# Kernel optimization log

Measured on AMD Instinct MI355X. Metric: run time of the kernel, lower is better.

The kernel has to match this reference:

```python
import jax, jax.numpy as jnp
import numpy as np

N, E, H, C = 50000, 800000, 4, 32   # nodes, edges, heads, per-head channels
HID, LAT, G = H * C, 32, 128        # hidden, latent, num graphs
IN_DIM = 64
NEG_SLOPE = 0.2
BN_EPS = 1e-5


def setup_inputs() -> dict:
    key = jax.random.key(0)
    ks = jax.random.split(key, 20)
    inp = {
        "x": jax.random.normal(ks[0], (N, IN_DIM), jnp.float32),
        "edge_index": jax.random.randint(ks[1], (2, E), 0, N, jnp.int32),
        "batch": jnp.sort(jax.random.randint(ks[2], (N,), 0, G, jnp.int32)),
        # layer 0
        "W0": jax.random.normal(ks[3], (IN_DIM, HID), jnp.float32) * (1.0 / np.sqrt(IN_DIM)),
        "a_src0": jax.random.normal(ks[4], (H, C), jnp.float32) * 0.1,
        "a_dst0": jax.random.normal(ks[5], (H, C), jnp.float32) * 0.1,
        "b0": jnp.zeros((HID,), jnp.float32),
        # layer 1
        "W1": jax.random.normal(ks[6], (HID, HID), jnp.float32) * (1.0 / np.sqrt(HID)),
        "a_src1": jax.random.normal(ks[7], (H, C), jnp.float32) * 0.1,
        "a_dst1": jax.random.normal(ks[8], (H, C), jnp.float32) * 0.1,
        "b1": jnp.zeros((HID,), jnp.float32),
        # layer 2
        "W2": jax.random.normal(ks[9], (HID, HID), jnp.float32) * (1.0 / np.sqrt(HID)),
        "a_src2": jax.random.normal(ks[10], (H, C), jnp.float32) * 0.1,
        "a_dst2": jax.random.normal(ks[11], (H, C), jnp.float32) * 0.1,
        "b2": jnp.zeros((HID,), jnp.float32),
        # head
        "fc_w": jax.random.normal(ks[12], (HID, LAT), jnp.float32) * (1.0 / np.sqrt(HID)),
        "fc_b": jnp.zeros((LAT,), jnp.float32),
        "bn_g": jnp.ones((LAT,), jnp.float32),
        "bn_b": jnp.zeros((LAT,), jnp.float32),
    }
    return inp


def _gat_conv(x, src, dst, W, a_src, a_dst, b):
    n = x.shape[0]
    h = (x @ W).reshape(n, H, C)                      # [N,H,C]
    alpha_s = jnp.einsum("nhc,hc->nh", h, a_src)       # [N,H]
    alpha_d = jnp.einsum("nhc,hc->nh", h, a_dst)
    e = jax.nn.leaky_relu(alpha_s[src] + alpha_d[dst], NEG_SLOPE)  # [E',H]
    # scatter-softmax over incoming edges of each dst node
    m = jax.ops.segment_max(e, dst, num_segments=n)
    m = jnp.where(jnp.isfinite(m), m, 0.0)
    ex = jnp.exp(e - m[dst])
    denom = jax.ops.segment_sum(ex, dst, num_segments=n)
    alpha = ex / (denom[dst] + 1e-16)                  # [E',H]
    out = jax.ops.segment_sum(alpha[:, :, None] * h[src], dst, num_segments=n)
    return out.reshape(n, H * C) + b


def reference(x, edge_index, batch, W0, a_src0, a_dst0, b0, W1, a_src1, a_dst1, b1,
              W2, a_src2, a_dst2, b2, fc_w, fc_b, bn_g, bn_b):
    # PyG GATConv default add_self_loops=True
    loop = jnp.arange(N, dtype=edge_index.dtype)
    src = jnp.concatenate([edge_index[0], loop])
    dst = jnp.concatenate([edge_index[1], loop])

    h = x
    for (W, a_s, a_d, b) in ((W0, a_src0, a_dst0, b0),
                             (W1, a_src1, a_dst1, b1),
                             (W2, a_src2, a_dst2, b2)):
        h = _gat_conv(h, src, dst, W, a_s, a_d, b)
        h = jax.nn.leaky_relu(h, NEG_SLOPE)  # dropout is identity in eval

    pooled = jax.ops.segment_sum(h, batch, num_segments=G)  # global_add_pool -> [G,HID]
    out = pooled @ fc_w + fc_b
    # BatchNorm1d in eval mode with running_mean=0, running_var=1
    out = bn_g * out * (1.0 / np.sqrt(1.0 + BN_EPS)) + bn_b
    return out
```

## Files before the change

kernel.cpp:

```cpp
#include <hip/hip_runtime.h>
#include <hip/hip_bf16.h>
#include <float.h>

#define NEG 0.2f
#define SEGSHIFT 13
#define KE 24

__device__ __forceinline__ float leaky(float x) { return x > 0.0f ? x : NEG * x; }

__device__ __forceinline__ unsigned short f2bf(float f) {
  unsigned x = __float_as_uint(f);
  unsigned r = (x + 0x7fffu + ((x >> 16) & 1u)) >> 16;
  return (unsigned short)r;
}

__device__ __forceinline__ float2 bf2f2(unsigned u) {
  float2 r;
  r.x = __uint_as_float(u << 16);
  r.y = __uint_as_float(u & 0xffff0000u);
  return r;
}

using frag8 = __attribute__((ext_vector_type(8))) short;
using f32x4v = __attribute__((ext_vector_type(4))) float;

__global__ void zero_kernel(int* __restrict__ p, int n) {
  int i = blockIdx.x * blockDim.x + threadIdx.x;
  int stride = gridDim.x * blockDim.x;
  for (; i < n; i += stride) p[i] = 0;
}

__global__ void wcvt_kernel(const float* __restrict__ W, unsigned short* __restrict__ Wt, int K) {
  int i = blockIdx.x * 256 + threadIdx.x;
  if (i >= K * 128) return;
  int k = i >> 7, n = i & 127;
  Wt[n * K + k] = f2bf(W[i]);
}

__global__ void count_kernel(const int* __restrict__ ei, int* __restrict__ degseg,
                             int E, int N, int nseg) {
  int i = blockIdx.x * blockDim.x + threadIdx.x;
  if (i >= E + N) return;
  int src, dst;
  if (i < E) { src = ei[i]; dst = ei[E + i]; } else { src = dst = i - E; }
  atomicAdd(&degseg[(size_t)dst * nseg + (src >> SEGSHIFT)], 1);
}

__global__ __launch_bounds__(1024) void scan_block_kernel(const int* __restrict__ deg,
                                                          int* __restrict__ row_start,
                                                          int* __restrict__ sums, int n) {
  __shared__ int buf[1024];
  int t = threadIdx.x;
  int idx = blockIdx.x * 1024 + t;
  int x = (idx < n) ? deg[idx] : 0;
  int v = x;
  buf[t] = v;
  __syncthreads();
  for (int off = 1; off < 1024; off <<= 1) {
    int a = (t >= off) ? buf[t - off] : 0;
    __syncthreads();
    v += a;
    buf[t] = v;
    __syncthreads();
  }
  if (idx < n) row_start[idx] = v - x;
  if (t == 1023) sums[blockIdx.x] = v;
}

__global__ __launch_bounds__(1024) void scan_sums_kernel(int* __restrict__ sums,
                                                         int* __restrict__ row_start,
                                                         int nch, int n) {
  __shared__ int buf[1024];
  int t = threadIdx.x;
  int x = (t < nch) ? sums[t] : 0;
  int v = x;
  buf[t] = v;
  __syncthreads();
  for (int off = 1; off < 1024; off <<= 1) {
    int a = (t >= off) ? buf[t - off] : 0;
    __syncthreads();
    v += a;
    buf[t] = v;
    __syncthreads();
  }
  if (t < nch) sums[t] = v - x;
  if (t == 1023) row_start[n] = v;
}

__global__ __launch_bounds__(1024) void scan_add_kernel(int* __restrict__ row_start,
                                                        const int* __restrict__ sums, int n) {
  int idx = blockIdx.x * 1024 + threadIdx.x;
  if (idx < n) row_start[idx] += sums[blockIdx.x];
}

__global__ void fill_kernel(const int* __restrict__ ei, int* __restrict__ cursor,
                            const int* __restrict__ rowseg, int* __restrict__ csr_src,
                            int E, int N, int nseg) {
  int i = blockIdx.x * blockDim.x + threadIdx.x;
  if (i >= E + N) return;
  int src, dst;
  if (i < E) { src = ei[i]; dst = ei[E + i]; } else { src = dst = i - E; }
  size_t b = (size_t)dst * nseg + (src >> SEGSHIFT);
  int pos = atomicAdd(&cursor[b], 1);
  csr_src[rowseg[b] + pos] = src;
}

template <int FP32IN>
__global__ __launch_bounds__(256) void gemm_kernel(const void* __restrict__ Xin,
                                                   const unsigned short* __restrict__ Wtg,
                                                   unsigned short* __restrict__ Hb,
                                                   const float* __restrict__ a_src,
                                                   const float* __restrict__ a_dst,
                                                   float* __restrict__ as_arr,
                                                   float* __restrict__ ad_arr,
                                                   int nrows, int K) {
  __shared__ unsigned short Wt[128][136];
  __shared__ unsigned short Xs[64][136];
  int t = threadIdx.x;
  int wave = t >> 6, lane = t & 63;
  int n0 = lane & 15, quad = lane >> 4;
  int row0 = blockIdx.x * 64, wrow = wave * 16;

  for (int idx = t; idx < (K * 128) / 8; idx += 256) {
    int n = idx / (K >> 3), c8 = idx % (K >> 3);
    *(uint4*)(&Wt[n][c8 * 8]) = *(const uint4*)(Wtg + (size_t)n * K + c8 * 8);
  }
  int rowElems = K >> 3;
  if (FP32IN) {
    const float* Xf = (const float*)Xin;
    for (int idx = t; idx < 64 * K; idx += 256) {
      int r = idx / K, k = idx % K;
      int gr = row0 + r;
      Xs[r][k] = f2bf(gr < nrows ? Xf[(size_t)gr * K + k] : 0.f);
    }
  } else {
    const unsigned short* Xb = (const unsigned short*)Xin;
    for (int idx = t; idx < 64 * rowElems; idx += 256) {
      int r = idx / rowElems, c8 = idx % rowElems;
      int gr = row0 + r;
      uint4 v = make_uint4(0, 0, 0, 0);
      if (gr < nrows) v = *(const uint4*)(Xb + (size_t)gr * K + c8 * 8);
      *(uint4*)(&Xs[r][c8 * 8]) = v;
    }
  }
  __syncthreads();

  f32x4v acc[8];
#pragma unroll
  for (int c = 0; c < 8; ++c) acc[c] = (f32x4v){0.f, 0.f, 0.f, 0.f};

  for (int kb = 0; kb < K; kb += 32) {
    frag8 a = *(const frag8*)(&Xs[wrow + n0][kb + quad * 8]);
#pragma unroll
    for (int c = 0; c < 8; ++c) {
      frag8 b = *(const frag8*)(&Wt[c * 16 + n0][kb + quad * 8]);
      acc[c] = __builtin_amdgcn_mfma_f32_16x16x32_bf16(a, b, acc[c], 0, 0, 0);
    }
  }

  float asv[8], adv[8];
#pragma unroll
  for (int c = 0; c < 8; ++c) {
    asv[c] = a_src[c * 16 + n0];
    adv[c] = a_dst[c * 16 + n0];
  }
#pragma unroll
  for (int r = 0; r < 4; ++r) {
    float ps[4] = {0.f, 0.f, 0.f, 0.f}, pd[4] = {0.f, 0.f, 0.f, 0.f};
#pragma unroll
    for (int c = 0; c < 8; ++c) {
      int h = c >> 1;
      ps[h] += acc[c][r] * asv[c];
      pd[h] += acc[c][r] * adv[c];
    }
#pragma unroll
    for (int off = 1; off < 16; off <<= 1) {
#pragma unroll
      for (int h = 0; h < 4; ++h) {
        ps[h] += __shfl_xor(ps[h], off);
        pd[h] += __shfl_xor(pd[h], off);
      }
    }
    if (n0 == 0) {
      int m = row0 + wrow + quad * 4 + r;
      if (m < nrows) {
#pragma unroll
        for (int h = 0; h < 4; ++h) {
          as_arr[(size_t)m * 4 + h] = ps[h];
          ad_arr[(size_t)m * 4 + h] = pd[h];
        }
      }
    }
  }

  __syncthreads();
#pragma unroll
  for (int c = 0; c < 8; ++c)
#pragma unroll
    for (int r = 0; r < 4; ++r)
      Xs[wrow + quad * 4 + r][c * 16 + n0] = f2bf(acc[c][r]);
  __syncthreads();
  for (int idx = t; idx < 64 * 16; idx += 256) {
    int r = idx >> 4, c8 = idx & 15;
    int gr = row0 + r;
    if (gr < nrows)
      *(uint4*)(Hb + (size_t)gr * 128 + c8 * 8) = *(const uint4*)(&Xs[r][c8 * 8]);
  }
}

template <int POOL>
__global__ __launch_bounds__(256) void agg_kernel(const unsigned short* __restrict__ Hb,
                                                  const float* __restrict__ as_arr,
                                                  const float* __restrict__ ad_arr,
                                                  const int* __restrict__ csr_src,
                                                  const int* __restrict__ rowseg,
                                                  const float* __restrict__ bias,
                                                  unsigned short* __restrict__ xnext,
                                                  const int* __restrict__ batch,
                                                  float* __restrict__ pooled,
                                                  int N, int nseg) {
  __shared__ __align__(16) char rowbuf[4][KE * 256];
  __shared__ __align__(16) float e_lds[4][KE][4];
  int wid = threadIdx.x >> 6;
  int lane = threadIdx.x & 63;
  int n = blockIdx.x * 4 + wid;
  if (n >= N) return;
  int rs = rowseg[(size_t)n * nseg];
  int re = rowseg[(size_t)n * nseg + nseg];
  int l16 = lane & 15;
  int sub = lane >> 4;
  int head = l16 >> 2;

  float4 ad4 = *(const float4*)(ad_arr + (size_t)n * 4);
  char* myrows = rowbuf[wid];

  float4 dsum = make_float4(0.f, 0.f, 0.f, 0.f);
  float acc[8];
#pragma unroll
  for (int c = 0; c < 8; ++c) acc[c] = 0.f;

  for (int base = rs; base < re; base += KE) {
    asm volatile("s_waitcnt lgkmcnt(0)" ::: "memory");

    int sj = 0;
    float4 e4 = make_float4(0.f, 0.f, 0.f, 0.f);
    if (lane < KE && base + lane < re) {
      sj = csr_src[base + lane];
      float4 a4 = *(const float4*)(as_arr + (size_t)sj * 4);
      e4.x = __expf(fminf(leaky(a4.x + ad4.x), 80.f));
      e4.y = __expf(fminf(leaky(a4.y + ad4.y), 80.f));
      e4.z = __expf(fminf(leaky(a4.z + ad4.z), 80.f));
      e4.w = __expf(fminf(leaky(a4.w + ad4.w), 80.f));
      dsum.x += e4.x; dsum.y += e4.y; dsum.z += e4.z; dsum.w += e4.w;
    }
    if (lane < KE) *(float4*)(&e_lds[wid][lane][0]) = e4;

#pragma unroll
    for (int j = 0; j < KE; ++j) {
      int sju = __builtin_amdgcn_readlane(sj, j);
      const char* gp = (const char*)Hb + (size_t)(unsigned)sju * 256 + lane * 4;
      __builtin_amdgcn_global_load_lds(
          (const __attribute__((address_space(1))) void*)gp,
          (__attribute__((address_space(3))) void*)(myrows + j * 256), 4, 0, 0);
    }
    asm volatile("s_waitcnt vmcnt(0) lgkmcnt(0)" ::: "memory");
    __builtin_amdgcn_sched_barrier(0);

#pragma unroll
    for (int j = 0; j < KE; j += 4) {
      float w = e_lds[wid][j + sub][head];
      uint4 u = *(const uint4*)(myrows + (j + sub) * 256 + l16 * 16);
      float2 f;
      f = bf2f2(u.x); acc[0] += w * f.x; acc[1] += w * f.y;
      f = bf2f2(u.y); acc[2] += w * f.x; acc[3] += w * f.y;
      f = bf2f2(u.z); acc[4] += w * f.x; acc[5] += w * f.y;
      f = bf2f2(u.w); acc[6] += w * f.x; acc[7] += w * f.y;
    }
  }

#pragma unroll
  for (int c = 0; c < 8; ++c) acc[c] += __shfl_xor(acc[c], 16);
#pragma unroll
  for (int c = 0; c < 8; ++c) acc[c] += __shfl_xor(acc[c], 32);

#pragma unroll
  for (int off = 1; off < 64; off <<= 1) {
    dsum.x += __shfl_xor(dsum.x, off);
    dsum.y += __shfl_xor(dsum.y, off);
    dsum.z += __shfl_xor(dsum.z, off);
    dsum.w += __shfl_xor(dsum.w, off);
  }
  float denom = (head == 0) ? dsum.x : (head == 1) ? dsum.y : (head == 2) ? dsum.z : dsum.w;
  float inv = 1.0f / (denom + 1e-16f);

  if (POOL) {
    int g = batch[n];
    float p0 = 0.f, p1 = 0.f;
    switch (sub) {
      case 0: p0 = acc[0]; p1 = acc[1]; break;
      case 1: p0 = acc[2]; p1 = acc[3]; break;
      case 2: p0 = acc[4]; p1 = acc[5]; break;
      case 3: p0 = acc[6]; p1 = acc[7]; break;
    }
    int ch = 8 * l16 + 2 * sub;
    float v0 = leaky(p0 * inv + bias[ch]);
    float v1 = leaky(p1 * inv + bias[ch + 1]);
    atomicAdd(&pooled[(size_t)g * 128 + ch], v0);
    atomicAdd(&pooled[(size_t)g * 128 + ch + 1], v1);
  } else {
    if (sub == 0) {
      float4 bv0 = *(const float4*)(bias + 8 * l16);
      float4 bv1 = *(const float4*)(bias + 8 * l16 + 4);
      float v0 = leaky(acc[0] * inv + bv0.x);
      float v1 = leaky(acc[1] * inv + bv0.y);
      float v2 = leaky(acc[2] * inv + bv0.z);
      float v3 = leaky(acc[3] * inv + bv0.w);
      float v4 = leaky(acc[4] * inv + bv1.x);
      float v5 = leaky(acc[5] * inv + bv1.y);
      float v6 = leaky(acc[6] * inv + bv1.z);
      float v7 = leaky(acc[7] * inv + bv1.w);
      uint4 pk;
      pk.x = ((unsigned)f2bf(v1) << 16) | (unsigned)f2bf(v0);
      pk.y = ((unsigned)f2bf(v3) << 16) | (unsigned)f2bf(v2);
      pk.z = ((unsigned)f2bf(v5) << 16) | (unsigned)f2bf(v4);
      pk.w = ((unsigned)f2bf(v7) << 16) | (unsigned)f2bf(v6);
      ((uint4*)xnext)[(size_t)n * 16 + l16] = pk;
    }
  }
}

__global__ void head_kernel(const float* __restrict__ pooled, const float* __restrict__ fc_w,
                            const float* __restrict__ fc_b, const float* __restrict__ bn_g,
                            const float* __restrict__ bn_b, float* __restrict__ out, int G) {
  int t = threadIdx.x;
  int g = blockIdx.x * 8 + (t >> 5);
  int j = t & 31;
  if (g >= G) return;
  const float* pr = pooled + (size_t)g * 128;
  float acc = 0.f;
#pragma unroll 8
  for (int k = 0; k < 128; ++k) acc += pr[k] * fc_w[k * 32 + j];
  const float inv = 0.9999950000374997f;
  out[g * 32 + j] = bn_g[j] * (acc + fc_b[j]) * inv + bn_b[j];
}

extern "C" void kernel_launch(void* const* d_in, const int* in_sizes, int n_in,
                              void* d_out, int out_size, void* d_ws, size_t ws_size,
                              hipStream_t stream) {
  const float* x = (const float*)d_in[0];
  const int* ei = (const int*)d_in[1];
  const int* batch = (const int*)d_in[2];
  const float* Wm[3] = {(const float*)d_in[3], (const float*)d_in[7], (const float*)d_in[11]};
  const float* a_s[3] = {(const float*)d_in[4], (const float*)d_in[8], (const float*)d_in[12]};
  const float* a_d[3] = {(const float*)d_in[5], (const float*)d_in[9], (const float*)d_in[13]};
  const float* bb[3] = {(const float*)d_in[6], (const float*)d_in[10], (const float*)d_in[14]};
  const float* fc_w = (const float*)d_in[15];
  const float* fc_b = (const float*)d_in[16];
  const float* bn_g = (const float*)d_in[17];
  const float* bn_b = (const float*)d_in[18];
  float* out = (float*)d_out;

  int N = in_sizes[0] / 64;
  int E = in_sizes[1] / 2;
  int G = out_size / 32;
  int Etot = E + N;
  int nseg = ((N - 1) >> SEGSHIFT) + 1;
  int L = N * nseg;

  char* p = (char*)d_ws;
  auto carve = [&](size_t bytes) {
    char* r = p;
    p += (bytes + 255) & ~size_t(255);
    return r;
  };
  int* degseg    = (int*)carve((size_t)L * 4);
  int* cursor    = (int*)carve((size_t)L * 4);
  float* pooled  = (float*)carve((size_t)G * 128 * 4);
  int* rowseg    = (int*)carve((size_t)(L + 1) * 4);
  int* sums      = (int*)carve(4096);
  int* csr_src   = (int*)carve((size_t)Etot * 4);
  unsigned short* Hb  = (unsigned short*)carve((size_t)N * 128 * 2);
  unsigned short* Xb  = (unsigned short*)carve((size_t)N * 128 * 2);
  unsigned short* Wt0 = (unsigned short*)carve(64 * 128 * 2);
  unsigned short* Wt1 = (unsigned short*)carve(128 * 128 * 2);
  unsigned short* Wt2 = (unsigned short*)carve(128 * 128 * 2);
  float* as_arr  = (float*)carve((size_t)N * 4 * 4);
  float* ad_arr  = (float*)carve((size_t)N * 4 * 4);

  int nz = (int)(((char*)(pooled + (size_t)G * 128) - (char*)degseg) / 4);
  zero_kernel<<<512, 256, 0, stream>>>(degseg, nz);

  wcvt_kernel<<<(64 * 128 + 255) / 256, 256, 0, stream>>>(Wm[0], Wt0, 64);
  wcvt_kernel<<<(128 * 128 + 255) / 256, 256, 0, stream>>>(Wm[1], Wt1, 128);
  wcvt_kernel<<<(128 * 128 + 255) / 256, 256, 0, stream>>>(Wm[2], Wt2, 128);

  int egrid = (Etot + 255) / 256;
  count_kernel<<<egrid, 256, 0, stream>>>(ei, degseg, E, N, nseg);
  int nch = (L + 1023) / 1024;
  scan_block_kernel<<<nch, 1024, 0, stream>>>(degseg, rowseg, sums, L);
  scan_sums_kernel<<<1, 1024, 0, stream>>>(sums, rowseg, nch, L);
  scan_add_kernel<<<nch, 1024, 0, stream>>>(rowseg, sums, L);
  fill_kernel<<<egrid, 256, 0, stream>>>(ei, cursor, rowseg, csr_src, E, N, nseg);

  int ggrid = (N + 63) / 64;
  int ngrid = (N + 3) / 4;

  gemm_kernel<1><<<ggrid, 256, 0, stream>>>(x, Wt0, Hb, a_s[0], a_d[0], as_arr, ad_arr, N, 64);
  agg_kernel<0><<<ngrid, 256, 0, stream>>>(Hb, as_arr, ad_arr, csr_src, rowseg, bb[0],
                                           Xb, nullptr, nullptr, N, nseg);
  gemm_kernel<0><<<ggrid, 256, 0, stream>>>(Xb, Wt1, Hb, a_s[1], a_d[1], as_arr, ad_arr, N, 128);
  agg_kernel<0><<<ngrid, 256, 0, stream>>>(Hb, as_arr, ad_arr, csr_src, rowseg, bb[1],
                                           Xb, nullptr, nullptr, N, nseg);
  gemm_kernel<0><<<ggrid, 256, 0, stream>>>(Xb, Wt2, Hb, a_s[2], a_d[2], as_arr, ad_arr, N, 128);
  agg_kernel<1><<<ngrid, 256, 0, stream>>>(Hb, as_arr, ad_arr, csr_src, rowseg, bb[2],
                                           nullptr, batch, pooled, N, nseg);

  head_kernel<<<(G + 7) / 8, 256, 0, stream>>>(pooled, fc_w, fc_b, bn_g, bn_b, out, G);
}
```

Before: 502.3 us.

## Replace LDS-staged row gathers with direct vector loads in GAT aggregation

The aggregation kernel stops staging neighbour feature rows into shared memory with global_load_lds and per-batch waitcnt barriers. Each wave now walks 16 edges at a time, broadcasts source indices and attention weights through lane shuffles, and issues four direct 16-byte global loads per lane. This removes the LDS traffic, the buffers and the full-drain waits. It also raises occupancy through a launch-bounds hint, at the cost of smaller batches per iteration and more shuffle instructions.

```diff
diff --git a/kernel.cpp b/kernel.cpp
--- a/kernel.cpp
+++ b/kernel.cpp
@@ -4,7 +4,6 @@
 
 #define NEG 0.2f
 #define SEGSHIFT 13
-#define KE 24
 
 __device__ __forceinline__ float leaky(float x) { return x > 0.0f ? x : NEG * x; }
 
@@ -208,19 +207,34 @@
   }
 }
 
+#define COMPG(E, U)                                                 \
+  do {                                                              \
+    float2 f_;                                                      \
+    f_ = bf2f2((U).x); acc[0] += (E) * f_.x; acc[1] += (E) * f_.y;  \
+    f_ = bf2f2((U).y); acc[2] += (E) * f_.x; acc[3] += (E) * f_.y;  \
+    f_ = bf2f2((U).z); acc[4] += (E) * f_.x; acc[5] += (E) * f_.y;  \
+    f_ = bf2f2((U).w); acc[6] += (E) * f_.x; acc[7] += (E) * f_.y;  \
+  } while (0)
+
+__device__ __forceinline__ float eselect(const float4& e4, int src, int head) {
+  float x = __shfl(e4.x, src);
+  float y = __shfl(e4.y, src);
+  float z = __shfl(e4.z, src);
+  float w = __shfl(e4.w, src);
+  return head == 0 ? x : head == 1 ? y : head == 2 ? z : w;
+}
+
 template <int POOL>
-__global__ __launch_bounds__(256) void agg_kernel(const unsigned short* __restrict__ Hb,
-                                                  const float* __restrict__ as_arr,
-                                                  const float* __restrict__ ad_arr,
-                                                  const int* __restrict__ csr_src,
-                                                  const int* __restrict__ rowseg,
-                                                  const float* __restrict__ bias,
-                                                  unsigned short* __restrict__ xnext,
-                                                  const int* __restrict__ batch,
-                                                  float* __restrict__ pooled,
-                                                  int N, int nseg) {
-  __shared__ __align__(16) char rowbuf[4][KE * 256];
-  __shared__ __align__(16) float e_lds[4][KE][4];
+__global__ __launch_bounds__(256, 4) void agg_kernel(const unsigned short* __restrict__ Hb,
+                                                     const float* __restrict__ as_arr,
+                                                     const float* __restrict__ ad_arr,
+                                                     const int* __restrict__ csr_src,
+                                                     const int* __restrict__ rowseg,
+                                                     const float* __restrict__ bias,
+                                                     unsigned short* __restrict__ xnext,
+                                                     const int* __restrict__ batch,
+                                                     float* __restrict__ pooled,
+                                                     int N, int nseg) {
   int wid = threadIdx.x >> 6;
   int lane = threadIdx.x & 63;
   int n = blockIdx.x * 4 + wid;
@@ -232,50 +246,42 @@
   int head = l16 >> 2;
 
   float4 ad4 = *(const float4*)(ad_arr + (size_t)n * 4);
-  char* myrows = rowbuf[wid];
+  const uint4* hb4 = (const uint4*)Hb;
 
   float4 dsum = make_float4(0.f, 0.f, 0.f, 0.f);
   float acc[8];
 #pragma unroll
   for (int c = 0; c < 8; ++c) acc[c] = 0.f;
 
-  for (int base = rs; base < re; base += KE) {
-    asm volatile("s_waitcnt lgkmcnt(0)" ::: "memory");
-
-    int sj = 0;
+  for (int i = rs; i < re; i += 16) {
+    int cnt = re - i;
+    int sld = 0;
     float4 e4 = make_float4(0.f, 0.f, 0.f, 0.f);
-    if (lane < KE && base + lane < re) {
-      sj = csr_src[base + lane];
-      float4 a4 = *(const float4*)(as_arr + (size_t)sj * 4);
+    if (lane < 16 && lane < cnt) {
+      sld = csr_src[i + lane];
+      float4 a4 = *(const float4*)(as_arr + (size_t)sld * 4);
       e4.x = __expf(fminf(leaky(a4.x + ad4.x), 80.f));
       e4.y = __expf(fminf(leaky(a4.y + ad4.y), 80.f));
       e4.z = __expf(fminf(leaky(a4.z + ad4.z), 80.f));
       e4.w = __expf(fminf(leaky(a4.w + ad4.w), 80.f));
       dsum.x += e4.x; dsum.y += e4.y; dsum.z += e4.z; dsum.w += e4.w;
     }
-    if (lane < KE) *(float4*)(&e_lds[wid][lane][0]) = e4;
-
-#pragma unroll
-    for (int j = 0; j < KE; ++j) {
-      int sju = __builtin_amdgcn_readlane(sj, j);
-      const char* gp = (const char*)Hb + (size_t)(unsigned)sju * 256 + lane * 4;
-      __builtin_amdgcn_global_load_lds(
-          (const __attribute__((address_space(1))) void*)gp,
-          (__attribute__((address_space(3))) void*)(myrows + j * 256), 4, 0, 0);
-    }
-    asm volatile("s_waitcnt vmcnt(0) lgkmcnt(0)" ::: "memory");
-    __builtin_amdgcn_sched_barrier(0);
-
-#pragma unroll
-    for (int j = 0; j < KE; j += 4) {
-      float w = e_lds[wid][j + sub][head];
-      uint4 u = *(const uint4*)(myrows + (j + sub) * 256 + l16 * 16);
-      float2 f;
-      f = bf2f2(u.x); acc[0] += w * f.x; acc[1] += w * f.y;
-      f = bf2f2(u.y); acc[2] += w * f.x; acc[3] += w * f.y;
-      f = bf2f2(u.z); acc[4] += w * f.x; acc[5] += w * f.y;
-      f = bf2f2(u.w); acc[6] += w * f.x; acc[7] += w * f.y;
-    }
+    int s0 = __shfl(sld, sub);
+    int s1 = __shfl(sld, 4 + sub);
+    int s2 = __shfl(sld, 8 + sub);
+    int s3 = __shfl(sld, 12 + sub);
+    uint4 u0 = hb4[(size_t)s0 * 16 + l16];
+    uint4 u1 = hb4[(size_t)s1 * 16 + l16];
+    uint4 u2 = hb4[(size_t)s2 * 16 + l16];
+    uint4 u3 = hb4[(size_t)s3 * 16 + l16];
+    float e0 = eselect(e4, sub, head);
+    float e1 = eselect(e4, 4 + sub, head);
+    float e2 = eselect(e4, 8 + sub, head);
+    float e3 = eselect(e4, 12 + sub, head);
+    COMPG(e0, u0);
+    COMPG(e1, u1);
+    COMPG(e2, u2);
+    COMPG(e3, u3);
   }
 
 #pragma unroll
@@ -329,6 +335,8 @@
   }
 }
 
+#undef COMPG
+
 __global__ void head_kernel(const float* __restrict__ pooled, const float* __restrict__ fc_w,
                             const float* __restrict__ fc_b, const float* __restrict__ bn_g,
                             const float* __restrict__ bn_b, float* __restrict__ out, int G) {
```

Result: faster. 480.2 us (-4.4%).
